# Optimization experiments

Hardware: AMD Instinct MI355X
Metric: run time of the kernel (lower is better)

Reference implementation:

```python
import jax, jax.numpy as jnp
import numpy as np

B, S, H = 2, 2048, 2048
NH, NKV, HD = 32, 8, 64
MAXP = 4096


def _apply_rope(x, cos, sin, positions):
    # x: [b, h, s, d]; cos/sin: [max_pos, d//2]; positions: [b, s]
    c = cos[positions][:, None]  # [b,1,s,d/2]
    s_ = sin[positions][:, None]
    x1 = x[..., ::2]
    x2 = x[..., 1::2]
    rotated = jnp.stack((-x2, x1), axis=-1).reshape(x.shape)  # interleave
    c2 = jnp.concatenate([c, c], axis=-1)   # repeat(1,1,1,2) tiling
    s2 = jnp.concatenate([s_, s_], axis=-1)
    return x * c2 + rotated * s2


def setup_inputs() -> dict:
    key = jax.random.key(0)
    ks = jax.random.split(key, 10)
    hidden_states = jax.random.normal(ks[0], (B, S, H), dtype=jnp.float32)
    # RoPE tables (use real rotary tables for realism)
    inv_freq = 1.0 / (10000.0 ** (jnp.arange(0, HD, 2, dtype=jnp.float32) / HD))
    t = jnp.arange(MAXP, dtype=jnp.float32)
    freqs = jnp.outer(t, inv_freq)  # [max_pos, d/2]
    cos = jnp.cos(freqs)
    sin = jnp.sin(freqs)
    positions = jnp.broadcast_to(jnp.arange(S, dtype=jnp.int32), (B, S))
    # additive causal mask
    neg = jnp.finfo(jnp.float32).min
    mask = jnp.where(jnp.tril(jnp.ones((S, S), dtype=bool)), 0.0, neg)[None, None]
    sc = 1.0 / np.sqrt(H)
    q_w = jax.random.normal(ks[1], (NH * HD, H), dtype=jnp.float32) * sc
    q_b = jnp.zeros((NH * HD,), dtype=jnp.float32)
    k_w = jax.random.normal(ks[2], (NKV * HD, H), dtype=jnp.float32) * sc
    k_b = jnp.zeros((NKV * HD,), dtype=jnp.float32)
    v_w = jax.random.normal(ks[3], (NKV * HD, H), dtype=jnp.float32) * sc
    v_b = jnp.zeros((NKV * HD,), dtype=jnp.float32)
    o_w = jax.random.normal(ks[4], (H, NH * HD), dtype=jnp.float32) * sc
    return {"hidden_states": hidden_states, "cos": cos, "sin": sin,
            "positions": positions, "mask": mask,
            "q_w": q_w, "q_b": q_b, "k_w": k_w, "k_b": k_b,
            "v_w": v_w, "v_b": v_b, "o_w": o_w}


def reference(hidden_states, cos, sin, positions, mask, q_w, q_b, k_w, k_b, v_w, v_b, o_w):
    bsz, seq_len, _ = hidden_states.shape
    groups = NH // NKV
    q = (hidden_states @ q_w.T + q_b).reshape(bsz, seq_len, NH, HD).transpose(0, 2, 1, 3)
    k = (hidden_states @ k_w.T + k_b).reshape(bsz, seq_len, NKV, HD).transpose(0, 2, 1, 3)
    v = (hidden_states @ v_w.T + v_b).reshape(bsz, seq_len, NKV, HD).transpose(0, 2, 1, 3)
    q = _apply_rope(q, cos, sin, positions)
    k = _apply_rope(k, cos, sin, positions)
    if groups > 1:
        k = jnp.repeat(k, groups, axis=1)
        v = jnp.repeat(v, groups, axis=1)
    scale = 1.0 / np.sqrt(HD)
    attn = jnp.einsum('bhqd,bhkd->bhqk', q, k) * scale
    attn = attn + mask
    attn = jax.nn.softmax(attn.astype(jnp.float32), axis=-1).astype(q.dtype)
    out = jnp.einsum('bhqk,bhkd->bhqd', attn, v)
    out = out.transpose(0, 2, 1, 3).reshape(bsz, seq_len, NH * HD)
    return out @ o_w.T
```

## Files before the change

kernel.cpp:

```cpp
#include <hip/hip_runtime.h>
#include <hip/hip_bf16.h>

#define BB   2
#define SS   2048
#define HH   2048
#define NH   32
#define NKV  8
#define HD   64
#define NTOK (BB * SS)
#define NQKV (NH * HD + 2 * NKV * HD)
#define KOFF (NH * HD)
#define VOFF (NH * HD + NKV * HD)

#define QSC  0.1803368801111244f

typedef short  short8  __attribute__((ext_vector_type(8)));
typedef short  short4v __attribute__((ext_vector_type(4)));
typedef float  float4v __attribute__((ext_vector_type(4)));

using bf16 = __hip_bfloat16;

#define DEV static __device__ __forceinline__

DEV short8 load8(const bf16* p) { return *(const short8*)p; }
DEV short8 load8s(const short* p) { return *(const short8*)p; }

DEV short f2bfbits(float f) {
    union { bf16 h; short s; } u;
    u.h = __float2bfloat16(f);
    return u.s;
}

DEV unsigned int packbf2(float a, float b) {
    return (unsigned int)(unsigned short)f2bfbits(a)
         | ((unsigned int)(unsigned short)f2bfbits(b) << 16);
}

DEV void async16(const bf16* g, short* l) {
    __builtin_amdgcn_global_load_lds(
        (const __attribute__((address_space(1))) unsigned int*)g,
        (__attribute__((address_space(3))) unsigned int*)l, 16, 0, 0);
}

__global__ __launch_bounds__(256) void cvt_all_kernel(
    const float* __restrict__ hidden, const float* __restrict__ q_w,
    const float* __restrict__ k_w, const float* __restrict__ v_w,
    const float* __restrict__ o_w,
    bf16* __restrict__ Hb, bf16* __restrict__ Wqkv, bf16* __restrict__ Wo) {
    int blk = blockIdx.x;
    const float* src;
    bf16* dst;
    int off;
    if (blk < 8192)       { src = hidden; dst = Hb;   off = blk * 1024; }
    else if (blk < 12288) { src = q_w; dst = Wqkv;    off = (blk - 8192) * 1024; }
    else if (blk < 13312) { src = k_w; dst = Wqkv + (size_t)KOFF * HH; off = (blk - 12288) * 1024; }
    else if (blk < 14336) { src = v_w; dst = Wqkv + (size_t)VOFF * HH; off = (blk - 13312) * 1024; }
    else                  { src = o_w; dst = Wo;      off = (blk - 14336) * 1024; }
    int i = off + threadIdx.x * 4;
    float4 v = *(const float4*)(src + i);
    short4v o;
    o[0] = f2bfbits(v.x); o[1] = f2bfbits(v.y);
    o[2] = f2bfbits(v.z); o[3] = f2bfbits(v.w);
    *(short4v*)(dst + i) = o;
}
#define CVT_BLOCKS 18432

struct GemmCtx {
    const bf16 *gA, *gB;
    short *lA, *lB;
    const short *rdA, *rdB;
    int p0;
};

DEV void gemm_setup(GemmCtx& c, const bf16* A, const bf16* Bw, int K,
                    int m0, int n0, short* As, short* Bs) {
    int lane = threadIdx.x & 63, w = threadIdx.x >> 6;
    int quad = lane >> 4, tq = lane & 15;
    int srow = lane >> 3;
    int schunk = (lane & 7) ^ srow;
    c.gA = A  + (size_t)(m0 + w * 32 + srow) * K + schunk * 8;
    c.gB = Bw + (size_t)(n0 + w * 32 + srow) * K + schunk * 8;
    c.lA = As + (w * 32) * 64;
    c.lB = Bs + (w * 32) * 64;
    int mbase = (w >> 1) * 64, nbase = (w & 1) * 64;
    c.rdA = As + (mbase + tq) * 64;
    c.rdB = Bs + (nbase + tq) * 64;
    c.p0 = (quad ^ (tq & 7)) * 8;
}

DEV void gemm_mainloop(GemmCtx& c, int K, float4v acc[4][4]) {
    for (int k0 = 0; k0 < K; k0 += 64) {
        __syncthreads();
#pragma unroll
        for (int cc = 0; cc < 4; ++cc) {
            async16(c.gA + (size_t)cc * 8 * K + k0, c.lA + cc * 8 * 64);
            async16(c.gB + (size_t)cc * 8 * K + k0, c.lB + cc * 8 * 64);
        }
        __syncthreads();
#pragma unroll
        for (int kh = 0; kh < 2; ++kh) {
            int off = c.p0 ^ (kh * 32);
            short8 af[4], bfr[4];
#pragma unroll
            for (int mi = 0; mi < 4; ++mi) af[mi]  = load8s(c.rdA + mi * 16 * 64 + off);
#pragma unroll
            for (int nj = 0; nj < 4; ++nj) bfr[nj] = load8s(c.rdB + nj * 16 * 64 + off);
#pragma unroll
            for (int mi = 0; mi < 4; ++mi)
#pragma unroll
                for (int nj = 0; nj < 4; ++nj)
                    acc[mi][nj] = __builtin_amdgcn_mfma_f32_16x16x32_bf16(
                        af[mi], bfr[nj], acc[mi][nj], 0, 0, 0);
        }
    }
}

__global__ __launch_bounds__(256, 3) void qkv_kernel(
    const bf16* __restrict__ Hb, const bf16* __restrict__ Wqkv,
    const float* __restrict__ qbias, const float* __restrict__ kbias,
    const float* __restrict__ vbias,
    const float* __restrict__ cosp, const float* __restrict__ sinp,
    const int* __restrict__ posp,
    bf16* __restrict__ Qb, bf16* __restrict__ Kb, bf16* __restrict__ Vt) {
    __shared__ __align__(16) short As[128 * 64];
    __shared__ __align__(16) short Bs[128 * 64];
    int lane = threadIdx.x & 63, w = threadIdx.x >> 6;
    int quad = lane >> 4, tq = lane & 15;
    int m0 = blockIdx.y * 128, n0 = blockIdx.x * 128;
    int mbase = (w >> 1) * 64, nbase = (w & 1) * 64;

    GemmCtx c;
    gemm_setup(c, Hb, Wqkv, HH, m0, n0, As, Bs);
    float4v acc[4][4] = {};
    gemm_mainloop(c, HH, acc);

    float biasv[4];
#pragma unroll
    for (int nj = 0; nj < 4; ++nj) {
        int colg = n0 + nbase + nj * 16 + tq;
        biasv[nj] = (colg < KOFF) ? qbias[colg]
                  : (colg < VOFF) ? kbias[colg - KOFF] : vbias[colg - VOFF];
    }

#pragma unroll
    for (int mi = 0; mi < 4; ++mi) {
#pragma unroll
        for (int r = 0; r < 4; ++r) {
            int tok = m0 + mbase + mi * 16 + quad * 4 + r;
            int p = posp[tok];
#pragma unroll
            for (int nj = 0; nj < 4; ++nj) {
                int colg = n0 + nbase + nj * 16 + tq;
                float val = acc[mi][nj][r] + biasv[nj];
                if (colg < VOFF) {
                    float pv = __shfl_xor(val, 1);
                    int jh = colg & 63;
                    float Cv = cosp[p * 32 + (jh & 31)];
                    float Sv = sinp[p * 32 + (jh & 31)];
                    float outv = (jh & 1) ? (val * Cv + pv * Sv)
                                          : (val * Cv - pv * Sv);
                    if (colg < KOFF)
                        Qb[(size_t)tok * (NH * HD) + colg] = __float2bfloat16(outv * QSC);
                    else
                        Kb[(size_t)tok * (NKV * HD) + (colg - KOFF)] = __float2bfloat16(outv);
                } else {
                    int c2 = colg - VOFF;
                    int kv = c2 >> 6, d = c2 & 63;
                    int bb = tok >> 11, s = tok & (SS - 1);
                    Vt[(((size_t)bb * NKV + kv) * HD + d) * SS + s] = __float2bfloat16(val);
                }
            }
        }
    }
}

__global__ __launch_bounds__(256, 3) void oproj_kernel(
    const bf16* __restrict__ AO, const bf16* __restrict__ Wo,
    float* __restrict__ out) {
    __shared__ __align__(16) short As[128 * 64];
    __shared__ __align__(16) short Bs[128 * 64];
    int lane = threadIdx.x & 63, w = threadIdx.x >> 6;
    int quad = lane >> 4, tq = lane & 15;
    int m0 = blockIdx.y * 128, n0 = blockIdx.x * 128;
    int mbase = (w >> 1) * 64, nbase = (w & 1) * 64;

    GemmCtx c;
    gemm_setup(c, AO, Wo, NH * HD, m0, n0, As, Bs);
    float4v acc[4][4] = {};
    gemm_mainloop(c, NH * HD, acc);

#pragma unroll
    for (int mi = 0; mi < 4; ++mi) {
#pragma unroll
        for (int nj = 0; nj < 4; ++nj) {
            int colg = n0 + nbase + nj * 16 + tq;
#pragma unroll
            for (int r = 0; r < 4; ++r) {
                int tok = m0 + mbase + mi * 16 + quad * 4 + r;
                out[(size_t)tok * HH + colg] = acc[mi][nj][r];
            }
        }
    }
}

#define PST 72

template<bool MASK>
DEV void attn_kv_step(int kv0, int qw0, int qw1, int w, int lane, int quad, int tq,
                      const bf16* __restrict__ Kg, const bf16* __restrict__ Vg,
                      short* Ks, short* Vs, short* myp,
                      const short8 (&aq)[2][2], float4v (&ot)[4][2], float (&ls)[2]) {
    int srow = lane >> 3;
    int schunk = (lane & 7) ^ srow;

    __syncthreads();
#pragma unroll
    for (int cc = 0; cc < 2; ++cc) {
        int rl = w * 16 + cc * 8;
        async16(Kg + (size_t)(kv0 + rl + srow) * (NKV * HD) + schunk * 8,
                Ks + rl * 64);
        async16(Vg + (size_t)(rl + srow) * SS + kv0 + schunk * 8,
                Vs + rl * 64);
    }
    __syncthreads();

    int p0 = (quad ^ (tq & 7)) * 8;

#pragma unroll
    for (int t = 0; t < 4; ++t) {
        const short* kr = Ks + (t * 16 + tq) * 64;
        short8 k0 = load8s(kr + p0);
        short8 k1 = load8s(kr + (p0 ^ 32));
        float4v s0 = {0.f, 0.f, 0.f, 0.f};
        float4v s1 = {0.f, 0.f, 0.f, 0.f};
        s0 = __builtin_amdgcn_mfma_f32_16x16x32_bf16(k0, aq[0][0], s0, 0, 0, 0);
        s0 = __builtin_amdgcn_mfma_f32_16x16x32_bf16(k1, aq[0][1], s0, 0, 0, 0);
        s1 = __builtin_amdgcn_mfma_f32_16x16x32_bf16(k0, aq[1][0], s1, 0, 0, 0);
        s1 = __builtin_amdgcn_mfma_f32_16x16x32_bf16(k1, aq[1][1], s1, 0, 0, 0);
#pragma unroll
        for (int qc = 0; qc < 2; ++qc) {
            const float4v& s = qc ? s1 : s0;
            int qw = qc ? qw1 : qw0;
            float p[4];
#pragma unroll
            for (int r = 0; r < 4; ++r) {
                float e = __builtin_amdgcn_exp2f(s[r]);
                if (MASK) {
                    int kvg = kv0 + t * 16 + quad * 4 + r;
                    e = (kvg <= qw) ? e : 0.f;
                }
                p[r] = e;
                ls[qc] += e;
            }
            int pos = (qc * 16 + tq) * PST + t * 16 + quad * 4;
            *(unsigned int*)(myp + pos)     = packbf2(p[0], p[1]);
            *(unsigned int*)(myp + pos + 2) = packbf2(p[2], p[3]);
        }
    }

    short8 pf00 = load8s(myp + tq * PST + quad * 8);
    short8 pf01 = load8s(myp + tq * PST + 32 + quad * 8);
    short8 pf10 = load8s(myp + (16 + tq) * PST + quad * 8);
    short8 pf11 = load8s(myp + (16 + tq) * PST + 32 + quad * 8);

#pragma unroll
    for (int i = 0; i < 4; ++i) {
        const short* vr = Vs + (i * 16 + tq) * 64;
        short8 bv0 = load8s(vr + p0);
        short8 bv1 = load8s(vr + (p0 ^ 32));
        ot[i][0] = __builtin_amdgcn_mfma_f32_16x16x32_bf16(bv0, pf00, ot[i][0], 0, 0, 0);
        ot[i][0] = __builtin_amdgcn_mfma_f32_16x16x32_bf16(bv1, pf01, ot[i][0], 0, 0, 0);
        ot[i][1] = __builtin_amdgcn_mfma_f32_16x16x32_bf16(bv0, pf10, ot[i][1], 0, 0, 0);
        ot[i][1] = __builtin_amdgcn_mfma_f32_16x16x32_bf16(bv1, pf11, ot[i][1], 0, 0, 0);
    }
}

DEV void attn_superblock(int sb, int b, int h, int w, int lane, int quad, int tq,
                         const bf16* __restrict__ Qb,
                         const bf16* __restrict__ Kg, const bf16* __restrict__ Vg,
                         short* Ks, short* Vs, short* myp, bf16* __restrict__ AO) {
    int qw0 = sb + w * 32 + tq;
    int qw1 = qw0 + 16;
    const bf16* Qr0 = Qb + (size_t)(b * SS + qw0) * (NH * HD) + h * HD + quad * 8;
    const bf16* Qr1 = Qr0 + (size_t)16 * (NH * HD);
    short8 aq[2][2];
    aq[0][0] = load8(Qr0); aq[0][1] = load8(Qr0 + 32);
    aq[1][0] = load8(Qr1); aq[1][1] = load8(Qr1 + 32);

    float4v ot[4][2] = {};
    float ls[2] = {0.f, 0.f};

    for (int kv0 = 0; kv0 < sb; kv0 += 64)
        attn_kv_step<false>(kv0, qw0, qw1, w, lane, quad, tq, Kg, Vg, Ks, Vs, myp,
                            aq, ot, ls);
    attn_kv_step<true>(sb, qw0, qw1, w, lane, quad, tq, Kg, Vg, Ks, Vs, myp,
                       aq, ot, ls);
    attn_kv_step<true>(sb + 64, qw0, qw1, w, lane, quad, tq, Kg, Vg, Ks, Vs, myp,
                       aq, ot, ls);

#pragma unroll
    for (int qc = 0; qc < 2; ++qc) {
        float lsum = ls[qc];
        lsum += __shfl_xor(lsum, 16);
        lsum += __shfl_xor(lsum, 32);
        float inv = 1.0f / lsum;
        int qg = qc ? qw1 : qw0;
        bf16* obase = AO + (size_t)(b * SS + qg) * (NH * HD) + h * HD + quad * 4;
#pragma unroll
        for (int i = 0; i < 4; ++i) {
            short4v o;
#pragma unroll
            for (int r = 0; r < 4; ++r) o[r] = f2bfbits(ot[i][qc][r] * inv);
            *(short4v*)(obase + i * 16) = o;
        }
    }
}

__global__ __launch_bounds__(256, 2) void attn_kernel(
    const bf16* __restrict__ Qb, const bf16* __restrict__ Kb,
    const bf16* __restrict__ Vt, bf16* __restrict__ AO) {
    __shared__ __align__(16) short Ks[64 * 64];
    __shared__ __align__(16) short Vs[64 * 64];
    __shared__ __align__(16) short plds[4][32 * PST];

    int lane = threadIdx.x & 63, w = threadIdx.x >> 6;
    int quad = lane >> 4, tq = lane & 15;

    int x = blockIdx.x;
    int xcd = x & 7, xi = x >> 3;
    int pair = xcd * 2 + (xi & 1);
    int b = pair >> 3, kvh = pair & 7;
    int h = kvh * 4 + (xi >> 1);

    const bf16* Kg = Kb + (size_t)(b * SS) * (NKV * HD) + kvh * HD;
    const bf16* Vg = Vt + (size_t)((b * NKV + kvh) * HD) * SS;
    short* myp = &plds[w][0];

    int jq = blockIdx.y;
    attn_superblock((15 - jq) * 128, b, h, w, lane, quad, tq, Qb, Kg, Vg, Ks, Vs, myp, AO);
    attn_superblock(jq * 128,        b, h, w, lane, quad, tq, Qb, Kg, Vg, Ks, Vs, myp, AO);
}

extern "C" void kernel_launch(void* const* d_in, const int* in_sizes, int n_in,
                              void* d_out, int out_size, void* d_ws, size_t ws_size,
                              hipStream_t stream) {
    const float* hidden = (const float*)d_in[0];
    const float* cosp   = (const float*)d_in[1];
    const float* sinp   = (const float*)d_in[2];
    const int*   posp   = (const int*)d_in[3];
    const float* q_w = (const float*)d_in[5];
    const float* q_b = (const float*)d_in[6];
    const float* k_w = (const float*)d_in[7];
    const float* k_b = (const float*)d_in[8];
    const float* v_w = (const float*)d_in[9];
    const float* v_b = (const float*)d_in[10];
    const float* o_w = (const float*)d_in[11];
    float* out = (float*)d_out;

    char* ws = (char*)d_ws;
    bf16* Hb   = (bf16*)ws; ws += (size_t)NTOK * HH * 2;
    bf16* Wqkv = (bf16*)ws; ws += (size_t)NQKV * HH * 2;
    bf16* Wo   = (bf16*)ws; ws += (size_t)HH * (NH * HD) * 2;
    bf16* Qb   = (bf16*)ws; ws += (size_t)NTOK * (NH * HD) * 2;
    bf16* Kb   = (bf16*)ws; ws += (size_t)NTOK * (NKV * HD) * 2;
    bf16* Vt   = (bf16*)ws; ws += (size_t)NTOK * (NKV * HD) * 2;
    bf16* AO   = (bf16*)ws; ws += (size_t)NTOK * (NH * HD) * 2;

    cvt_all_kernel<<<CVT_BLOCKS, 256, 0, stream>>>(
        hidden, q_w, k_w, v_w, o_w, Hb, Wqkv, Wo);

    qkv_kernel<<<dim3(NQKV / 128, NTOK / 128), 256, 0, stream>>>(
        Hb, Wqkv, q_b, k_b, v_b, cosp, sinp, posp, Qb, Kb, Vt);

    attn_kernel<<<dim3(64, 8), 256, 0, stream>>>(Qb, Kb, Vt, AO);

    oproj_kernel<<<dim3(HH / 128, NTOK / 128), 256, 0, stream>>>(AO, Wo, out);
}
```

Before: 316.5 us.

## Replace GEMM mainloop with 8-wave double-buffered pipelined 256-tile kernel

Replaces the single-buffered 128x128 GEMM used by the QKV and output projections with an 8-wave, 256-row tile GEMM. It double-buffers LDS, interleaves async global-to-LDS loads with four MFMA quadrants, and uses explicit waitcnt, barriers and setprio to overlap memory with compute. Blocks are remapped to a flat grid with an XCD-aware swizzle. The aim is to hide load latency and raise tile reuse, at the cost of more LDS and registers per block and lower occupancy.

```diff
diff --git a/kernel.cpp b/kernel.cpp
--- a/kernel.cpp
+++ b/kernel.cpp
@@ -65,92 +65,159 @@
 }
 #define CVT_BLOCKS 18432
 
-struct GemmCtx {
-    const bf16 *gA, *gB;
-    short *lA, *lB;
-    const short *rdA, *rdB;
-    int p0;
-};
-
-DEV void gemm_setup(GemmCtx& c, const bf16* A, const bf16* Bw, int K,
-                    int m0, int n0, short* As, short* Bs) {
-    int lane = threadIdx.x & 63, w = threadIdx.x >> 6;
-    int quad = lane >> 4, tq = lane & 15;
-    int srow = lane >> 3;
-    int schunk = (lane & 7) ^ srow;
-    c.gA = A  + (size_t)(m0 + w * 32 + srow) * K + schunk * 8;
-    c.gB = Bw + (size_t)(n0 + w * 32 + srow) * K + schunk * 8;
-    c.lA = As + (w * 32) * 64;
-    c.lB = Bs + (w * 32) * 64;
-    int mbase = (w >> 1) * 64, nbase = (w & 1) * 64;
-    c.rdA = As + (mbase + tq) * 64;
-    c.rdB = Bs + (nbase + tq) * 64;
-    c.p0 = (quad ^ (tq & 7)) * 8;
-}
-
-DEV void gemm_mainloop(GemmCtx& c, int K, float4v acc[4][4]) {
-    for (int k0 = 0; k0 < K; k0 += 64) {
-        __syncthreads();
-#pragma unroll
-        for (int cc = 0; cc < 4; ++cc) {
-            async16(c.gA + (size_t)cc * 8 * K + k0, c.lA + cc * 8 * 64);
-            async16(c.gB + (size_t)cc * 8 * K + k0, c.lB + cc * 8 * 64);
-        }
-        __syncthreads();
-#pragma unroll
-        for (int kh = 0; kh < 2; ++kh) {
-            int off = c.p0 ^ (kh * 32);
-            short8 af[4], bfr[4];
-#pragma unroll
-            for (int mi = 0; mi < 4; ++mi) af[mi]  = load8s(c.rdA + mi * 16 * 64 + off);
-#pragma unroll
-            for (int nj = 0; nj < 4; ++nj) bfr[nj] = load8s(c.rdB + nj * 16 * 64 + off);
-#pragma unroll
-            for (int mi = 0; mi < 4; ++mi)
-#pragma unroll
-                for (int nj = 0; nj < 4; ++nj)
-                    acc[mi][nj] = __builtin_amdgcn_mfma_f32_16x16x32_bf16(
-                        af[mi], bfr[nj], acc[mi][nj], 0, 0, 0);
-        }
-    }
-}
-
-__global__ __launch_bounds__(256, 3) void qkv_kernel(
+
+#define QUAD(mh, nh) \
+    { _Pragma("unroll") \
+      for (int kh = 0; kh < 2; ++kh) { \
+        _Pragma("unroll") \
+        for (int mi = 0; mi < 4; ++mi) { \
+          _Pragma("unroll") \
+          for (int nq = 0; nq < NFN / 2; ++nq) \
+            acc[(mh) * 4 + mi][(nh) * (NFN / 2) + nq] = \
+                __builtin_amdgcn_mfma_f32_16x16x32_bf16( \
+                    afr[(mh) * 4 + mi][kh], bfr[(nh) * (NFN / 2) + nq][kh], \
+                    acc[(mh) * 4 + mi][(nh) * (NFN / 2) + nq], 0, 0, 0); } } }
+
+#define STA(buf, r0, kt) async16(gA + (size_t)(r0) * K + (kt) * 64, lA + (buf) * ASZ + (r0) * 64)
+#define STB(buf, r0, kt) async16(gB + (size_t)(r0) * K + (kt) * 64, lB + (buf) * BSZ + (r0) * 64)
+
+template<int NFN, int K>
+DEV void gemm8_loop(const bf16* __restrict__ A, const bf16* __restrict__ Bw,
+                    int m0, int n0, short* sA, short* sB,
+                    float4v (&acc)[8][NFN]) {
+    constexpr int NT    = K / 64;
+    constexpr int ASZ   = 256 * 64;
+    constexpr int BROWS = NFN * 64;
+    constexpr int BSZ   = BROWS * 64;
+    constexpr int VN    = (NFN == 4) ? 6 : 4;
+
+    const int lane = threadIdx.x & 63, w = threadIdx.x >> 6;
+    const int quad = lane >> 4, tq = lane & 15;
+    const int wm = w >> 2, wn = w & 3;
+    const int srow = lane >> 3;
+    const int schunk = (lane & 7) ^ srow;
+
+    const bf16* gA = A  + (size_t)(m0 + w * 8 + srow) * K + schunk * 8;
+    const bf16* gB = Bw + (size_t)(n0 + w * 8 + srow) * K + schunk * 8;
+    short* lA = sA + w * 8 * 64;
+    short* lB = sB + w * 8 * 64;
+
+    STB(0, 0, 0);          if (NFN == 4) STB(0, 64, 0);
+    STB(0, BROWS / 2, 0);  if (NFN == 4) STB(0, BROWS / 2 + 64, 0);
+    STA(0, 0, 0);   STA(0, 64, 0);
+    STA(0, 128, 0); STA(0, 192, 0);
+    STB(1, 0, 1);          if (NFN == 4) STB(1, 64, 1);
+    STB(1, BROWS / 2, 1);  if (NFN == 4) STB(1, BROWS / 2 + 64, 1);
+    STA(1, 0, 1);   STA(1, 64, 1);
+    asm volatile("s_waitcnt vmcnt(%0)" :: "i"(VN) : "memory");
+    __builtin_amdgcn_s_barrier();
+
+    const int p0 = (quad ^ (tq & 7)) * 8;
+
+    for (int t = 0; t < NT; ++t) {
+        const int buf = t & 1;
+        const short* rA = sA + buf * ASZ + (wm * 128 + tq) * 64;
+        const short* rB = sB + buf * BSZ + (wn * (NFN * 16) + tq) * 64;
+        short8 afr[8][2];
+        short8 bfr[NFN][2];
+        const bool st1 = (t + 1 < NT);
+        const bool st2 = (t + 2 < NT);
+
+#pragma unroll
+        for (int mi = 0; mi < 4; ++mi) {
+            afr[mi][0] = load8s(rA + mi * 16 * 64 + p0);
+            afr[mi][1] = load8s(rA + mi * 16 * 64 + (p0 ^ 32));
+        }
+#pragma unroll
+        for (int nj = 0; nj < NFN; ++nj) {
+            bfr[nj][0] = load8s(rB + nj * 16 * 64 + p0);
+            bfr[nj][1] = load8s(rB + nj * 16 * 64 + (p0 ^ 32));
+        }
+        if (st1) { STA((t + 1) & 1, 128, t + 1); STA((t + 1) & 1, 192, t + 1); }
+        __builtin_amdgcn_s_barrier();
+        asm volatile("s_waitcnt lgkmcnt(0)" ::: "memory");
+        __builtin_amdgcn_sched_barrier(0);
+        __builtin_amdgcn_s_setprio(1);
+        QUAD(0, 0);
+        __builtin_amdgcn_s_setprio(0);
+        __builtin_amdgcn_s_barrier();
+
+#pragma unroll
+        for (int mi = 4; mi < 8; ++mi) {
+            afr[mi][0] = load8s(rA + mi * 16 * 64 + p0);
+            afr[mi][1] = load8s(rA + mi * 16 * 64 + (p0 ^ 32));
+        }
+        if (st2) { STB(buf, 0, t + 2); if (NFN == 4) STB(buf, 64, t + 2); }
+        __builtin_amdgcn_s_barrier();
+        asm volatile("s_waitcnt lgkmcnt(0)" ::: "memory");
+        __builtin_amdgcn_sched_barrier(0);
+        __builtin_amdgcn_s_setprio(1);
+        QUAD(0, 1);
+        __builtin_amdgcn_s_setprio(0);
+        __builtin_amdgcn_s_barrier();
+
+        if (st2) { STB(buf, BROWS / 2, t + 2); if (NFN == 4) STB(buf, BROWS / 2 + 64, t + 2); }
+        __builtin_amdgcn_s_barrier();
+        asm volatile("s_waitcnt lgkmcnt(0)" ::: "memory");
+        __builtin_amdgcn_sched_barrier(0);
+        __builtin_amdgcn_s_setprio(1);
+        QUAD(1, 0);
+        __builtin_amdgcn_s_setprio(0);
+        __builtin_amdgcn_s_barrier();
+
+        if (st2) { STA(buf, 0, t + 2); STA(buf, 64, t + 2); }
+        __builtin_amdgcn_s_barrier();
+        asm volatile("s_waitcnt lgkmcnt(0)" ::: "memory");
+        __builtin_amdgcn_sched_barrier(0);
+        __builtin_amdgcn_s_setprio(1);
+        QUAD(1, 1);
+        __builtin_amdgcn_s_setprio(0);
+        if (st2) asm volatile("s_waitcnt vmcnt(%0)" :: "i"(VN) : "memory");
+        else     asm volatile("s_waitcnt vmcnt(0)" ::: "memory");
+        __builtin_amdgcn_s_barrier();
+    }
+}
+
+__global__ __launch_bounds__(512, 2) void qkv8_kernel(
     const bf16* __restrict__ Hb, const bf16* __restrict__ Wqkv,
     const float* __restrict__ qbias, const float* __restrict__ kbias,
     const float* __restrict__ vbias,
     const float* __restrict__ cosp, const float* __restrict__ sinp,
     const int* __restrict__ posp,
     bf16* __restrict__ Qb, bf16* __restrict__ Kb, bf16* __restrict__ Vt) {
-    __shared__ __align__(16) short As[128 * 64];
-    __shared__ __align__(16) short Bs[128 * 64];
+    __shared__ __align__(16) short sA[2 * 256 * 64];
+    __shared__ __align__(16) short sB[2 * 256 * 64];
+
+    constexpr int NBN = NQKV / 256;
+    int flat = blockIdx.x;
+    int wg = (flat & 7) * 24 + (flat >> 3);
+    int bm = wg / NBN, bn = wg - bm * NBN;
+    int m0 = bm * 256, n0 = bn * 256;
+
+    float4v acc[8][4] = {};
+    gemm8_loop<4, HH>(Hb, Wqkv, m0, n0, sA, sB, acc);
+
     int lane = threadIdx.x & 63, w = threadIdx.x >> 6;
     int quad = lane >> 4, tq = lane & 15;
-    int m0 = blockIdx.y * 128, n0 = blockIdx.x * 128;
-    int mbase = (w >> 1) * 64, nbase = (w & 1) * 64;
-
-    GemmCtx c;
-    gemm_setup(c, Hb, Wqkv, HH, m0, n0, As, Bs);
-    float4v acc[4][4] = {};
-    gemm_mainloop(c, HH, acc);
+    int wm = w >> 2, wn = w & 3;
 
     float biasv[4];
 #pragma unroll
     for (int nj = 0; nj < 4; ++nj) {
-        int colg = n0 + nbase + nj * 16 + tq;
+        int colg = n0 + wn * 64 + nj * 16 + tq;
         biasv[nj] = (colg < KOFF) ? qbias[colg]
                   : (colg < VOFF) ? kbias[colg - KOFF] : vbias[colg - VOFF];
     }
 
 #pragma unroll
-    for (int mi = 0; mi < 4; ++mi) {
+    for (int mi = 0; mi < 8; ++mi) {
 #pragma unroll
         for (int r = 0; r < 4; ++r) {
-            int tok = m0 + mbase + mi * 16 + quad * 4 + r;
+            int tok = m0 + wm * 128 + mi * 16 + quad * 4 + r;
             int p = posp[tok];
 #pragma unroll
             for (int nj = 0; nj < 4; ++nj) {
-                int colg = n0 + nbase + nj * 16 + tq;
+                int colg = n0 + wn * 64 + nj * 16 + tq;
                 float val = acc[mi][nj][r] + biasv[nj];
                 if (colg < VOFF) {
                     float pv = __shfl_xor(val, 1);
@@ -174,29 +241,32 @@
     }
 }
 
-__global__ __launch_bounds__(256, 3) void oproj_kernel(
+__global__ __launch_bounds__(512, 2) void oproj8_kernel(
     const bf16* __restrict__ AO, const bf16* __restrict__ Wo,
     float* __restrict__ out) {
-    __shared__ __align__(16) short As[128 * 64];
-    __shared__ __align__(16) short Bs[128 * 64];
+    __shared__ __align__(16) short sA[2 * 256 * 64];
+    __shared__ __align__(16) short sB[2 * 128 * 64];
+
+    int flat = blockIdx.x;
+    int wg = (flat & 7) * 32 + (flat >> 3);
+    int bm = wg >> 4, bn = wg & 15;
+    int m0 = bm * 256, n0 = bn * 128;
+
+    float4v acc[8][2] = {};
+    gemm8_loop<2, NH * HD>(AO, Wo, m0, n0, sA, sB, acc);
+
     int lane = threadIdx.x & 63, w = threadIdx.x >> 6;
     int quad = lane >> 4, tq = lane & 15;
-    int m0 = blockIdx.y * 128, n0 = blockIdx.x * 128;
-    int mbase = (w >> 1) * 64, nbase = (w & 1) * 64;
-
-    GemmCtx c;
-    gemm_setup(c, AO, Wo, NH * HD, m0, n0, As, Bs);
-    float4v acc[4][4] = {};
-    gemm_mainloop(c, NH * HD, acc);
-
-#pragma unroll
-    for (int mi = 0; mi < 4; ++mi) {
-#pragma unroll
-        for (int nj = 0; nj < 4; ++nj) {
-            int colg = n0 + nbase + nj * 16 + tq;
+    int wm = w >> 2, wn = w & 3;
+
+#pragma unroll
+    for (int mi = 0; mi < 8; ++mi) {
+#pragma unroll
+        for (int nj = 0; nj < 2; ++nj) {
+            int colg = n0 + wn * 32 + nj * 16 + tq;
 #pragma unroll
             for (int r = 0; r < 4; ++r) {
-                int tok = m0 + mbase + mi * 16 + quad * 4 + r;
+                int tok = m0 + wm * 128 + mi * 16 + quad * 4 + r;
                 out[(size_t)tok * HH + colg] = acc[mi][nj][r];
             }
         }
@@ -369,10 +439,10 @@
     cvt_all_kernel<<<CVT_BLOCKS, 256, 0, stream>>>(
         hidden, q_w, k_w, v_w, o_w, Hb, Wqkv, Wo);
 
-    qkv_kernel<<<dim3(NQKV / 128, NTOK / 128), 256, 0, stream>>>(
+    qkv8_kernel<<<dim3(192), 512, 0, stream>>>(
         Hb, Wqkv, q_b, k_b, v_b, cosp, sinp, posp, Qb, Kb, Vt);
 
     attn_kernel<<<dim3(64, 8), 256, 0, stream>>>(Qb, Kb, Vt, AO);
 
-    oproj_kernel<<<dim3(HH / 128, NTOK / 128), 256, 0, stream>>>(AO, Wo, out);
-}
+    oproj8_kernel<<<dim3(256), 512, 0, stream>>>(AO, Wo, out);
+}
```

After: 346.3 us. 1.09x slower.

## Double-buffer attention K/V tiles and remap GEMM blocks for XCD locality

Applied to the files above, without the earlier changes.

The attention inner loop now prefetches the next 64-row K/V tile into a second LDS buffer while computing on the current one. It uses explicit vmcnt waits and raw barriers instead of a synchronous load-then-compute pattern, which is meant to hide global-load latency. Separately, the QKV and output-projection GEMMs switch to a 1D grid with an XCD-aware block remapping, so each XCD works on contiguous tiles and L2 reuse improves. The cost is double the K/V LDS footprint, which may hurt occupancy, plus handwritten waitcnt logic that depends on the exact count of outstanding loads.

```diff
diff --git a/kernel.cpp b/kernel.cpp
--- a/kernel.cpp
+++ b/kernel.cpp
@@ -126,7 +126,10 @@
     __shared__ __align__(16) short Bs[128 * 64];
     int lane = threadIdx.x & 63, w = threadIdx.x >> 6;
     int quad = lane >> 4, tq = lane & 15;
-    int m0 = blockIdx.y * 128, n0 = blockIdx.x * 128;
+    int flat = blockIdx.x;
+    int wg = (flat & 7) * 96 + (flat >> 3);
+    int bm = wg / 24, bn = wg % 24;
+    int m0 = bm * 128, n0 = bn * 128;
     int mbase = (w >> 1) * 64, nbase = (w & 1) * 64;
 
     GemmCtx c;
@@ -181,7 +184,10 @@
     __shared__ __align__(16) short Bs[128 * 64];
     int lane = threadIdx.x & 63, w = threadIdx.x >> 6;
     int quad = lane >> 4, tq = lane & 15;
-    int m0 = blockIdx.y * 128, n0 = blockIdx.x * 128;
+    int flat = blockIdx.x;
+    int wg = (flat & 7) * 64 + (flat >> 3);
+    int bm = wg >> 4, bn = wg & 15;
+    int m0 = bm * 128, n0 = bn * 128;
     int mbase = (w >> 1) * 64, nbase = (w & 1) * 64;
 
     GemmCtx c;
@@ -203,27 +209,29 @@
     }
 }
 
-#define PST 72
-
-template<bool MASK>
-DEV void attn_kv_step(int kv0, int qw0, int qw1, int w, int lane, int quad, int tq,
-                      const bf16* __restrict__ Kg, const bf16* __restrict__ Vg,
-                      short* Ks, short* Vs, short* myp,
-                      const short8 (&aq)[2][2], float4v (&ot)[4][2], float (&ls)[2]) {
+#define PST  72
+#define KVSZ (64 * 64)
+
+DEV void attn_stage(int buf, int kv0, int w, int lane,
+                    const bf16* __restrict__ Kg, const bf16* __restrict__ Vg,
+                    short* Ks, short* Vs) {
     int srow = lane >> 3;
     int schunk = (lane & 7) ^ srow;
-
-    __syncthreads();
 #pragma unroll
     for (int cc = 0; cc < 2; ++cc) {
         int rl = w * 16 + cc * 8;
         async16(Kg + (size_t)(kv0 + rl + srow) * (NKV * HD) + schunk * 8,
-                Ks + rl * 64);
+                Ks + buf * KVSZ + rl * 64);
         async16(Vg + (size_t)(rl + srow) * SS + kv0 + schunk * 8,
-                Vs + rl * 64);
-    }
-    __syncthreads();
-
+                Vs + buf * KVSZ + rl * 64);
+    }
+}
+
+template<bool MASK>
+DEV void attn_compute(int kv0, int qw0, int qw1, int quad, int tq,
+                      const short* __restrict__ Ks, const short* __restrict__ Vs,
+                      short* myp,
+                      const short8 (&aq)[2][2], float4v (&ot)[4][2], float (&ls)[2]) {
     int p0 = (quad ^ (tq & 7)) * 8;
 
 #pragma unroll
@@ -290,13 +298,27 @@
     float4v ot[4][2] = {};
     float ls[2] = {0.f, 0.f};
 
-    for (int kv0 = 0; kv0 < sb; kv0 += 64)
-        attn_kv_step<false>(kv0, qw0, qw1, w, lane, quad, tq, Kg, Vg, Ks, Vs, myp,
-                            aq, ot, ls);
-    attn_kv_step<true>(sb, qw0, qw1, w, lane, quad, tq, Kg, Vg, Ks, Vs, myp,
-                       aq, ot, ls);
-    attn_kv_step<true>(sb + 64, qw0, qw1, w, lane, quad, tq, Kg, Vg, Ks, Vs, myp,
-                       aq, ot, ls);
+    const int n = sb / 64 + 2;
+    attn_stage(0, 0, w, lane, Kg, Vg, Ks, Vs);
+
+    for (int i = 0; i < n; ++i) {
+        int kv0 = i * 64;
+        if (i + 1 < n) {
+            attn_stage((i + 1) & 1, kv0 + 64, w, lane, Kg, Vg, Ks, Vs);
+            asm volatile("s_waitcnt vmcnt(4)" ::: "memory");
+        } else {
+            asm volatile("s_waitcnt vmcnt(0)" ::: "memory");
+        }
+        __builtin_amdgcn_s_barrier();
+        const short* Kc = Ks + (i & 1) * KVSZ;
+        const short* Vc = Vs + (i & 1) * KVSZ;
+        if (kv0 < sb)
+            attn_compute<false>(kv0, qw0, qw1, quad, tq, Kc, Vc, myp, aq, ot, ls);
+        else
+            attn_compute<true>(kv0, qw0, qw1, quad, tq, Kc, Vc, myp, aq, ot, ls);
+        asm volatile("s_waitcnt lgkmcnt(0)" ::: "memory");
+        __builtin_amdgcn_s_barrier();
+    }
 
 #pragma unroll
     for (int qc = 0; qc < 2; ++qc) {
@@ -319,8 +341,8 @@
 __global__ __launch_bounds__(256, 2) void attn_kernel(
     const bf16* __restrict__ Qb, const bf16* __restrict__ Kb,
     const bf16* __restrict__ Vt, bf16* __restrict__ AO) {
-    __shared__ __align__(16) short Ks[64 * 64];
-    __shared__ __align__(16) short Vs[64 * 64];
+    __shared__ __align__(16) short Ks[2 * KVSZ];
+    __shared__ __align__(16) short Vs[2 * KVSZ];
     __shared__ __align__(16) short plds[4][32 * PST];
 
     int lane = threadIdx.x & 63, w = threadIdx.x >> 6;
@@ -369,10 +391,10 @@
     cvt_all_kernel<<<CVT_BLOCKS, 256, 0, stream>>>(
         hidden, q_w, k_w, v_w, o_w, Hb, Wqkv, Wo);
 
-    qkv_kernel<<<dim3(NQKV / 128, NTOK / 128), 256, 0, stream>>>(
+    qkv_kernel<<<dim3(768), 256, 0, stream>>>(
         Hb, Wqkv, q_b, k_b, v_b, cosp, sinp, posp, Qb, Kb, Vt);
 
     attn_kernel<<<dim3(64, 8), 256, 0, stream>>>(Qb, Kb, Vt, AO);
 
-    oproj_kernel<<<dim3(HH / 128, NTOK / 128), 256, 0, stream>>>(AO, Wo, out);
-}
+    oproj_kernel<<<dim3(512), 256, 0, stream>>>(AO, Wo, out);
+}
```

Result: faster. 304.6 us, median of 2 (-3.8%).
